# Optimization experiments

Hardware: AMD Instinct MI355X
Metric: run time of the kernel (lower is better)

The kernel has to match this reference:

```python
import jax, jax.numpy as jnp
import numpy as np

EPS = 1e-12  # F.normalize default eps


def _heatmap_pool(part_features, blocks):
    # part_features: [B, N, C]
    B, N, C = part_features.shape
    heatmap = jnp.mean(part_features, axis=-1)              # [B, N]
    arg = jnp.argsort(-heatmap, axis=1)                     # descending order
    x_sort = jnp.take_along_axis(part_features, arg[:, :, None], axis=1)  # [B, N, C]
    split_each = int(N / blocks)
    split_list = [split_each] * (blocks - 1)
    split_list.append(N - sum(split_list))
    offs = np.concatenate([[0], np.cumsum(split_list)])
    means = [jnp.mean(x_sort[:, offs[i]:offs[i + 1], :], axis=1) for i in range(blocks)]
    return jnp.stack(means, axis=2)                         # [B, C, blocks]


def _l2norm(x):
    n = jnp.sqrt(jnp.sum(x * x, axis=-1, keepdims=True))
    return x / jnp.maximum(n, EPS)


def setup_inputs() -> dict:
    key = jax.random.key(0)
    k1, k2 = jax.random.split(key)
    B, C, H, W = 64, 768, 24, 24
    return {
        "image_features1": jax.random.normal(k1, (B, C, H, W), dtype=jnp.float32),
        "image_features2": jax.random.normal(k2, (B, C, H, W), dtype=jnp.float32),
        "logit_scale": jnp.ones((1,), dtype=jnp.float32),
        "weights": jnp.ones((1,), dtype=jnp.float32),
        "blocks": 3,
    }


def reference(image_features1, image_features2, logit_scale, weights, blocks):
    B, C = image_features1.shape[0], image_features1.shape[1]
    f1 = image_features1.reshape(B, C, -1).transpose(0, 2, 1)  # [B, N, C]
    f2 = image_features2.reshape(B, C, -1).transpose(0, 2, 1)
    h1 = _heatmap_pool(f1, blocks)                             # [B, C, blocks]
    h2 = _heatmap_pool(f2, blocks)
    # cat blocks along channel dim: [B, C*blocks]
    b1 = jnp.concatenate([h1[:, :, i] for i in range(blocks)], axis=-1)
    b2 = jnp.concatenate([h2[:, :, i] for i in range(blocks)], axis=-1)
    n1 = _l2norm(b1)
    n2 = _l2norm(b2)
    return jnp.mean((n1 - n2) ** 2)
```

## Files before the change

kernel.cpp:

```cpp
#include <hip/hip_runtime.h>

#define NB 64
#define NC 768
#define NN 576
#define NF4 144
#define NCHUNK 8
#define CSZ 96
#define SPLIT 192

#define OFF_HM   0ull
#define SZ_HM    (2ull*NB*NCHUNK*NN*8ull)
#define OFF_GID  (OFF_HM + SZ_HM)
#define SZ_GID   (2ull*NB*NN*4ull)
#define OFF_GSUM (OFF_GID + SZ_GID)
#define SZ_GSUM  (2ull*NB*3ull*NC*4ull)
#define OFF_PB   (OFF_GSUM + SZ_GSUM)

__global__ __launch_bounds__(576) void k_heat(const float* __restrict__ f1,
                                              const float* __restrict__ f2,
                                              double* __restrict__ hm) {
    int bx    = blockIdx.x;
    int chunk = bx & (NCHUNK - 1);
    int b     = (bx >> 3) & (NB - 1);
    int inp   = bx >> 9;
    const float* f = inp ? f2 : f1;
    const float4* plane = (const float4*)(f + (size_t)b * NC * NN);

    int t  = threadIdx.x;
    int n4 = t % NF4;
    int cc = t / NF4;
    double a0 = 0, a1 = 0, a2 = 0, a3 = 0;
    int c0 = chunk * CSZ + cc;
    #pragma unroll 4
    for (int i = 0; i < CSZ / 4; ++i) {
        float4 v = plane[(size_t)(c0 + 4 * i) * NF4 + n4];
        a0 += (double)v.x; a1 += (double)v.y; a2 += (double)v.z; a3 += (double)v.w;
    }
    __shared__ double red[4][NN];
    red[cc][n4 * 4 + 0] = a0;
    red[cc][n4 * 4 + 1] = a1;
    red[cc][n4 * 4 + 2] = a2;
    red[cc][n4 * 4 + 3] = a3;
    __syncthreads();
    double s = red[0][t] + red[1][t] + red[2][t] + red[3][t];
    hm[((size_t)(inp * NB + b) * NCHUNK + chunk) * NN + t] = s;
}

__global__ __launch_bounds__(576) void k_rank(const double* __restrict__ hm,
                                              unsigned* __restrict__ gid) {
    int bx = blockIdx.x;
    int t  = threadIdx.x;
    const double* p = hm + (size_t)bx * NCHUNK * NN;
    double h = 0;
    #pragma unroll
    for (int ch = 0; ch < NCHUNK; ++ch) h += p[(size_t)ch * NN + t];
    __shared__ double hs[NN];
    hs[t] = h;
    __syncthreads();
    int cnt = 0;
    for (int j = 0; j < NN; ++j) {
        double hj = hs[j];
        cnt += (hj > h) ? 1 : ((hj == h && j < t) ? 1 : 0);
    }
    unsigned g = (cnt >= 2 * SPLIT) ? 2u : ((cnt >= SPLIT) ? 1u : 0u);
    gid[(size_t)bx * NN + t] = g;
}

__device__ __forceinline__ void acc3(float v, unsigned g,
                                     float& a0, float& a1, float& a2) {
    a0 += (g == 0u) ? v : 0.0f;
    a1 += (g == 1u) ? v : 0.0f;
    a2 += (g == 2u) ? v : 0.0f;
}

#define CG 48
__global__ __launch_bounds__(256) void k_gsum(const float* __restrict__ f1,
                                              const float* __restrict__ f2,
                                              const unsigned* __restrict__ gid,
                                              float* __restrict__ gsum) {
    int bx  = blockIdx.x;
    int cgi = bx & 15;
    int b   = (bx >> 4) & (NB - 1);
    int inp = bx >> 10;
    const float* f = inp ? f2 : f1;
    const float4* plane = (const float4*)(f + (size_t)b * NC * NN);
    const uint4* g4 = (const uint4*)(gid + (size_t)(inp * NB + b) * NN);
    float* out = gsum + (size_t)(inp * NB + b) * (3 * NC);

    int t = threadIdx.x;
    int w = t >> 6;
    int l = t & 63;

    uint4 ga = g4[l];
    uint4 gb = g4[l + 64];
    uint4 gc = make_uint4(0, 0, 0, 0);
    if (l < 16) gc = g4[l + 128];

    for (int i = 0; i < CG / 4; ++i) {
        int c = cgi * CG + 4 * i + w;
        const float4* row = plane + (size_t)c * NF4;
        float4 v0 = row[l];
        float4 v1 = row[l + 64];
        float4 v2 = make_float4(0.f, 0.f, 0.f, 0.f);
        if (l < 16) v2 = row[l + 128];

        float a0 = 0.f, a1 = 0.f, a2 = 0.f;
        acc3(v0.x, ga.x, a0, a1, a2); acc3(v0.y, ga.y, a0, a1, a2);
        acc3(v0.z, ga.z, a0, a1, a2); acc3(v0.w, ga.w, a0, a1, a2);
        acc3(v1.x, gb.x, a0, a1, a2); acc3(v1.y, gb.y, a0, a1, a2);
        acc3(v1.z, gb.z, a0, a1, a2); acc3(v1.w, gb.w, a0, a1, a2);
        acc3(v2.x, gc.x, a0, a1, a2); acc3(v2.y, gc.y, a0, a1, a2);
        acc3(v2.z, gc.z, a0, a1, a2); acc3(v2.w, gc.w, a0, a1, a2);

        #pragma unroll
        for (int m = 32; m; m >>= 1) {
            a0 += __shfl_xor(a0, m);
            a1 += __shfl_xor(a1, m);
            a2 += __shfl_xor(a2, m);
        }
        if (l == 0) {
            out[0 * NC + c] = a0;
            out[1 * NC + c] = a1;
            out[2 * NC + c] = a2;
        }
    }
}

__global__ __launch_bounds__(256) void k_mse(const float* __restrict__ gsum,
                                             double* __restrict__ pb) {
    int b = blockIdx.x;
    int t = threadIdx.x;
    int w = t >> 6, l = t & 63;
    const float* s1 = gsum + (size_t)b * (3 * NC);
    const float* s2 = gsum + (size_t)(NB + b) * (3 * NC);

    double v1[9], v2[9];
    double q1 = 0, q2 = 0;
    #pragma unroll
    for (int k = 0; k < 9; ++k) {
        int i = t + 256 * k;
        v1[k] = (double)s1[i] * (1.0 / 192.0);
        v2[k] = (double)s2[i] * (1.0 / 192.0);
        q1 += v1[k] * v1[k];
        q2 += v2[k] * v2[k];
    }
    #pragma unroll
    for (int m = 32; m; m >>= 1) { q1 += __shfl_xor(q1, m); q2 += __shfl_xor(q2, m); }
    __shared__ double red1[4], red2[4];
    if (l == 0) { red1[w] = q1; red2[w] = q2; }
    __syncthreads();
    q1 = red1[0] + red1[1] + red1[2] + red1[3];
    q2 = red2[0] + red2[1] + red2[2] + red2[3];
    double inv1 = 1.0 / fmax(sqrt(q1), 1e-12);
    double inv2 = 1.0 / fmax(sqrt(q2), 1e-12);

    double acc = 0;
    #pragma unroll
    for (int k = 0; k < 9; ++k) {
        double d = v1[k] * inv1 - v2[k] * inv2;
        acc += d * d;
    }
    #pragma unroll
    for (int m = 32; m; m >>= 1) acc += __shfl_xor(acc, m);
    __syncthreads();
    if (l == 0) red1[w] = acc;
    __syncthreads();
    if (t == 0) pb[b] = red1[0] + red1[1] + red1[2] + red1[3];
}

__global__ __launch_bounds__(64) void k_final(const double* __restrict__ pb,
                                              float* __restrict__ out) {
    int l = threadIdx.x;
    double v = pb[l];
    #pragma unroll
    for (int m = 32; m; m >>= 1) v += __shfl_xor(v, m);
    if (l == 0) out[0] = (float)(v / ((double)NB * 3.0 * (double)NC));
}

extern "C" void kernel_launch(void* const* d_in, const int* in_sizes, int n_in,
                              void* d_out, int out_size, void* d_ws, size_t ws_size,
                              hipStream_t stream) {
    (void)in_sizes; (void)n_in; (void)out_size; (void)ws_size;
    const float* f1 = (const float*)d_in[0];
    const float* f2 = (const float*)d_in[1];
    float* out = (float*)d_out;
    char* ws = (char*)d_ws;

    double*   hm   = (double*)(ws + OFF_HM);
    unsigned* gid  = (unsigned*)(ws + OFF_GID);
    float*    gsum = (float*)(ws + OFF_GSUM);
    double*   pb   = (double*)(ws + OFF_PB);

    k_heat <<<2 * NB * NCHUNK, 576, 0, stream>>>(f1, f2, hm);
    k_rank <<<2 * NB,          576, 0, stream>>>(hm, gid);
    k_gsum <<<2 * NB * (NC/CG),256, 0, stream>>>(f1, f2, gid, gsum);
    k_mse  <<<NB,              256, 0, stream>>>(gsum, pb);
    k_final<<<1,               64,  0, stream>>>(pb, out);
}
```

Before: 308.5 us.

## Restructure heat and group-sum kernels with byte group ids and partial sums

The heatmap kernel now has each of 192 threads sum three columns over 48 channels in 16 chunks, with no shared-memory reduction. Group ids are stored as bytes and read packed four per word. The group-sum kernel uses 16-lane sub-groups with prefix-style masks (all, >=1, ==2) and writes per-lane partials, which the MSE kernel sums. The aim is less shuffle-reduction and index traffic and better memory-level parallelism in the two bandwidth-bound passes over the inputs, at the cost of a larger partial-sum buffer.

```diff
diff --git a/kernel.cpp b/kernel.cpp
--- a/kernel.cpp
+++ b/kernel.cpp
@@ -4,56 +4,58 @@
 #define NC 768
 #define NN 576
 #define NF4 144
-#define NCHUNK 8
-#define CSZ 96
-#define SPLIT 192
+
+#define HCH 16
+#define HROWS 48
+#define GCH 8
+#define GROWS 96
 
 #define OFF_HM   0ull
-#define SZ_HM    (2ull*NB*NCHUNK*NN*8ull)
+#define SZ_HM    (2ull*NB*HCH*NN*8ull)
 #define OFF_GID  (OFF_HM + SZ_HM)
-#define SZ_GID   (2ull*NB*NN*4ull)
-#define OFF_GSUM (OFF_GID + SZ_GID)
-#define SZ_GSUM  (2ull*NB*3ull*NC*4ull)
-#define OFF_PB   (OFF_GSUM + SZ_GSUM)
+#define SZ_GID   (2ull*NB*NN)
+#define OFF_GP   (OFF_GID + SZ_GID)
+#define SZ_GP    (2ull*NB*NC*12ull*4ull)
+#define OFF_PB   (OFF_GP + SZ_GP)
 
-__global__ __launch_bounds__(576) void k_heat(const float* __restrict__ f1,
-                                              const float* __restrict__ f2,
-                                              double* __restrict__ hm) {
+__global__ __launch_bounds__(192, 6) void k_heat(const float* __restrict__ f1,
+                                                 const float* __restrict__ f2,
+                                                 double* __restrict__ hm) {
     int bx    = blockIdx.x;
-    int chunk = bx & (NCHUNK - 1);
-    int b     = (bx >> 3) & (NB - 1);
-    int inp   = bx >> 9;
-    const float* f = inp ? f2 : f1;
-    const float4* plane = (const float4*)(f + (size_t)b * NC * NN);
-
-    int t  = threadIdx.x;
-    int n4 = t % NF4;
-    int cc = t / NF4;
-    double a0 = 0, a1 = 0, a2 = 0, a3 = 0;
-    int c0 = chunk * CSZ + cc;
-    #pragma unroll 4
-    for (int i = 0; i < CSZ / 4; ++i) {
-        float4 v = plane[(size_t)(c0 + 4 * i) * NF4 + n4];
-        a0 += (double)v.x; a1 += (double)v.y; a2 += (double)v.z; a3 += (double)v.w;
+    int chunk = bx & (HCH - 1);
+    int b     = (bx >> 4) & (NB - 1);
+    int inp   = bx >> 10;
+    const float* f = (inp ? f2 : f1) + (size_t)b * NC * NN + (size_t)chunk * HROWS * NN;
+    int t = threadIdx.x;
+    double d0 = 0, d1 = 0, d2 = 0;
+    for (int r = 0; r < HROWS; r += 6) {
+        float v[18];
+        #pragma unroll
+        for (int rr = 0; rr < 6; ++rr) {
+            const float* row = f + (size_t)(r + rr) * NN + t;
+            v[rr * 3 + 0] = row[0];
+            v[rr * 3 + 1] = row[192];
+            v[rr * 3 + 2] = row[384];
+        }
+        #pragma unroll
+        for (int rr = 0; rr < 6; ++rr) {
+            d0 += (double)v[rr * 3 + 0];
+            d1 += (double)v[rr * 3 + 1];
+            d2 += (double)v[rr * 3 + 2];
+        }
     }
-    __shared__ double red[4][NN];
-    red[cc][n4 * 4 + 0] = a0;
-    red[cc][n4 * 4 + 1] = a1;
-    red[cc][n4 * 4 + 2] = a2;
-    red[cc][n4 * 4 + 3] = a3;
-    __syncthreads();
-    double s = red[0][t] + red[1][t] + red[2][t] + red[3][t];
-    hm[((size_t)(inp * NB + b) * NCHUNK + chunk) * NN + t] = s;
+    double* o = hm + ((size_t)(inp * NB + b) * HCH + chunk) * NN;
+    o[t] = d0; o[t + 192] = d1; o[t + 384] = d2;
 }
 
 __global__ __launch_bounds__(576) void k_rank(const double* __restrict__ hm,
-                                              unsigned* __restrict__ gid) {
+                                              unsigned char* __restrict__ gid8) {
     int bx = blockIdx.x;
     int t  = threadIdx.x;
-    const double* p = hm + (size_t)bx * NCHUNK * NN;
+    const double* p = hm + (size_t)bx * HCH * NN;
     double h = 0;
     #pragma unroll
-    for (int ch = 0; ch < NCHUNK; ++ch) h += p[(size_t)ch * NN + t];
+    for (int ch = 0; ch < HCH; ++ch) h += p[(size_t)ch * NN + t];
     __shared__ double hs[NN];
     hs[t] = h;
     __syncthreads();
@@ -62,85 +64,74 @@
         double hj = hs[j];
         cnt += (hj > h) ? 1 : ((hj == h && j < t) ? 1 : 0);
     }
-    unsigned g = (cnt >= 2 * SPLIT) ? 2u : ((cnt >= SPLIT) ? 1u : 0u);
-    gid[(size_t)bx * NN + t] = g;
+    gid8[(size_t)bx * NN + t] = (cnt >= 384) ? 2 : ((cnt >= 192) ? 1 : 0);
 }
 
-__device__ __forceinline__ void acc3(float v, unsigned g,
-                                     float& a0, float& a1, float& a2) {
-    a0 += (g == 0u) ? v : 0.0f;
-    a1 += (g == 1u) ? v : 0.0f;
-    a2 += (g == 2u) ? v : 0.0f;
-}
+__global__ __launch_bounds__(256, 4) void k_gsum(const float* __restrict__ f1,
+                                                 const float* __restrict__ f2,
+                                                 const unsigned* __restrict__ gidw,
+                                                 float* __restrict__ gp) {
+    int bx    = blockIdx.x;
+    int chunk = bx & (GCH - 1);
+    int b     = (bx >> 3) & (NB - 1);
+    int inp   = bx >> 9;
+    const float4* plane = (const float4*)((inp ? f2 : f1) + (size_t)b * NC * NN);
+    int t = threadIdx.x;
+    int w = t >> 6, l = t & 63;
+    int sub = l & 15, rr = l >> 4;
 
-#define CG 48
-__global__ __launch_bounds__(256) void k_gsum(const float* __restrict__ f1,
-                                              const float* __restrict__ f2,
-                                              const unsigned* __restrict__ gid,
-                                              float* __restrict__ gsum) {
-    int bx  = blockIdx.x;
-    int cgi = bx & 15;
-    int b   = (bx >> 4) & (NB - 1);
-    int inp = bx >> 10;
-    const float* f = inp ? f2 : f1;
-    const float4* plane = (const float4*)(f + (size_t)b * NC * NN);
-    const uint4* g4 = (const uint4*)(gid + (size_t)(inp * NB + b) * NN);
-    float* out = gsum + (size_t)(inp * NB + b) * (3 * NC);
+    unsigned g[9];
+    const unsigned* gw = gidw + (size_t)(inp * NB + b) * NF4;
+    #pragma unroll
+    for (int k = 0; k < 9; ++k) g[k] = gw[sub + 16 * k];
 
-    int t = threadIdx.x;
-    int w = t >> 6;
-    int l = t & 63;
-
-    uint4 ga = g4[l];
-    uint4 gb = g4[l + 64];
-    uint4 gc = make_uint4(0, 0, 0, 0);
-    if (l < 16) gc = g4[l + 128];
-
-    for (int i = 0; i < CG / 4; ++i) {
-        int c = cgi * CG + 4 * i + w;
-        const float4* row = plane + (size_t)c * NF4;
-        float4 v0 = row[l];
-        float4 v1 = row[l + 64];
-        float4 v2 = make_float4(0.f, 0.f, 0.f, 0.f);
-        if (l < 16) v2 = row[l + 128];
-
-        float a0 = 0.f, a1 = 0.f, a2 = 0.f;
-        acc3(v0.x, ga.x, a0, a1, a2); acc3(v0.y, ga.y, a0, a1, a2);
-        acc3(v0.z, ga.z, a0, a1, a2); acc3(v0.w, ga.w, a0, a1, a2);
-        acc3(v1.x, gb.x, a0, a1, a2); acc3(v1.y, gb.y, a0, a1, a2);
-        acc3(v1.z, gb.z, a0, a1, a2); acc3(v1.w, gb.w, a0, a1, a2);
-        acc3(v2.x, gc.x, a0, a1, a2); acc3(v2.y, gc.y, a0, a1, a2);
-        acc3(v2.z, gc.z, a0, a1, a2); acc3(v2.w, gc.w, a0, a1, a2);
-
+    float* out = gp + (size_t)(inp * NB + b) * NC * 12;
+    int cbase = chunk * GROWS + w * 4 + rr;
+    #pragma unroll 2
+    for (int i = 0; i < 6; ++i) {
+        int c = cbase + i * 16;
+        const float4* row = plane + (size_t)c * NF4 + sub;
+        float4 v[9];
         #pragma unroll
-        for (int m = 32; m; m >>= 1) {
-            a0 += __shfl_xor(a0, m);
-            a1 += __shfl_xor(a1, m);
-            a2 += __shfl_xor(a2, m);
+        for (int k = 0; k < 9; ++k) v[k] = row[16 * k];
+        float sa = 0.f, s1 = 0.f, s2 = 0.f;
+        #pragma unroll
+        for (int k = 0; k < 9; ++k) {
+            unsigned gwk = g[k];
+            float x;
+            unsigned gg;
+            x = v[k].x; gg = gwk & 0xffu;         sa += x; s1 += (gg >= 1u) ? x : 0.f; s2 += (gg == 2u) ? x : 0.f;
+            x = v[k].y; gg = (gwk >> 8) & 0xffu;  sa += x; s1 += (gg >= 1u) ? x : 0.f; s2 += (gg == 2u) ? x : 0.f;
+            x = v[k].z; gg = (gwk >> 16) & 0xffu; sa += x; s1 += (gg >= 1u) ? x : 0.f; s2 += (gg == 2u) ? x : 0.f;
+            x = v[k].w; gg = gwk >> 24;           sa += x; s1 += (gg >= 1u) ? x : 0.f; s2 += (gg == 2u) ? x : 0.f;
         }
-        if (l == 0) {
-            out[0 * NC + c] = a0;
-            out[1 * NC + c] = a1;
-            out[2 * NC + c] = a2;
+        sa += __shfl_xor(sa, 4); s1 += __shfl_xor(s1, 4); s2 += __shfl_xor(s2, 4);
+        sa += __shfl_xor(sa, 8); s1 += __shfl_xor(s1, 8); s2 += __shfl_xor(s2, 8);
+        if (sub < 4) {
+            float* o = out + (size_t)c * 12;
+            o[0 * 4 + sub] = sa - s1;
+            o[1 * 4 + sub] = s1 - s2;
+            o[2 * 4 + sub] = s2;
         }
     }
 }
 
-__global__ __launch_bounds__(256) void k_mse(const float* __restrict__ gsum,
+__global__ __launch_bounds__(256) void k_mse(const float* __restrict__ gp,
                                              double* __restrict__ pb) {
     int b = blockIdx.x;
     int t = threadIdx.x;
     int w = t >> 6, l = t & 63;
-    const float* s1 = gsum + (size_t)b * (3 * NC);
-    const float* s2 = gsum + (size_t)(NB + b) * (3 * NC);
+    const float4* s1 = (const float4*)(gp + (size_t)b * NC * 12);
+    const float4* s2 = (const float4*)(gp + (size_t)(NB + b) * NC * 12);
 
     double v1[9], v2[9];
     double q1 = 0, q2 = 0;
     #pragma unroll
     for (int k = 0; k < 9; ++k) {
-        int i = t + 256 * k;
-        v1[k] = (double)s1[i] * (1.0 / 192.0);
-        v2[k] = (double)s2[i] * (1.0 / 192.0);
+        int e = t + 256 * k;
+        float4 a = s1[e], c4 = s2[e];
+        v1[k] = ((double)a.x + (double)a.y + (double)a.z + (double)a.w) * (1.0 / 192.0);
+        v2[k] = ((double)c4.x + (double)c4.y + (double)c4.z + (double)c4.w) * (1.0 / 192.0);
         q1 += v1[k] * v1[k];
         q2 += v2[k] * v2[k];
     }
@@ -186,14 +177,14 @@
     float* out = (float*)d_out;
     char* ws = (char*)d_ws;
 
-    double*   hm   = (double*)(ws + OFF_HM);
-    unsigned* gid  = (unsigned*)(ws + OFF_GID);
-    float*    gsum = (float*)(ws + OFF_GSUM);
-    double*   pb   = (double*)(ws + OFF_PB);
+    double*        hm   = (double*)(ws + OFF_HM);
+    unsigned char* gid8 = (unsigned char*)(ws + OFF_GID);
+    float*         gp   = (float*)(ws + OFF_GP);
+    double*        pb   = (double*)(ws + OFF_PB);
 
-    k_heat <<<2 * NB * NCHUNK, 576, 0, stream>>>(f1, f2, hm);
-    k_rank <<<2 * NB,          576, 0, stream>>>(hm, gid);
-    k_gsum <<<2 * NB * (NC/CG),256, 0, stream>>>(f1, f2, gid, gsum);
-    k_mse  <<<NB,              256, 0, stream>>>(gsum, pb);
-    k_final<<<1,               64,  0, stream>>>(pb, out);
+    k_heat <<<2 * NB * HCH, 192, 0, stream>>>(f1, f2, hm);
+    k_rank <<<2 * NB,       576, 0, stream>>>(hm, gid8);
+    k_gsum <<<2 * NB * GCH, 256, 0, stream>>>(f1, f2, (const unsigned*)gid8, gp);
+    k_mse  <<<NB,           256, 0, stream>>>(gp, pb);
+    k_final<<<1,            64,  0, stream>>>(pb, out);
 }
```

Result: no change. 304.8 us (-1.2%).
